# Optimization experiments

Measured on AMD Instinct MI355X. Metric: run time of the kernel, lower is better.

Reference implementation:

```python
import jax, jax.numpy as jnp
import numpy as np

B, T, H = 8, 2048, 2048


def _wkv(key, value, time_decay, time_first):
    # key, value: [B, T, H]; time_decay/time_first: [H]
    u = time_first
    w = -jnp.exp(time_decay)  # negative decay per channel

    a0 = jnp.zeros(key.shape[::2], key.dtype)            # [B, H]
    b0 = jnp.zeros_like(a0)
    e0 = jnp.full_like(a0, -jnp.inf)

    def step(carry, kv):
        a, b, exponent = carry
        kt, vt = kv                                       # [B, H] each
        # output for this timestep (numerically stabilized)
        max_exp = jnp.maximum(exponent, u + kt)
        wt = jnp.exp(u + kt - max_exp)
        scale = jnp.exp(exponent - max_exp)
        wkv = (a * scale + wt * vt) / (b * scale + wt)
        # state update with decay w
        max_exp2 = jnp.maximum(exponent + w, kt)
        s1 = jnp.exp(exponent + w - max_exp2)
        s2 = jnp.exp(kt - max_exp2)
        a = s1 * a + s2 * vt
        b = s1 * b + s2
        return (a, b, max_exp2), wkv

    kT = jnp.swapaxes(key, 0, 1)    # [T, B, H] for scan over time
    vT = jnp.swapaxes(value, 0, 1)
    _, out = jax.lax.scan(step, (a0, b0, e0), (kT, vT))
    return jnp.swapaxes(out, 0, 1)  # [B, T, H]


def setup_inputs() -> dict:
    key = jax.random.key(0)
    k1, k2, k3, k4 = jax.random.split(key, 4)
    return {
        "key": jax.random.normal(k1, (B, T, H), jnp.float32),
        "value": jax.random.normal(k2, (B, T, H), jnp.float32),
        "time_decay": jax.random.normal(k3, (H,), jnp.float32) * 0.5,
        "time_first": jax.random.normal(k4, (H,), jnp.float32) * 0.5,
    }


def reference(key, value, time_decay, time_first):
    return _wkv(key, value, time_decay, time_first)
```

## Files before the change

kernel.cpp:

```cpp
#include <hip/hip_runtime.h>
#include <math.h>


#define TT 2048
#define HH 2048
#define BHc 16384
#define H4 512
#define NGRP 8

struct __align__(16) f4 { float v[4]; };

__device__ __forceinline__ void upd1(float& a, float& b, float& e,
                                     float w, float k, float vv) {
    float ew = e + w;
    float m  = fmaxf(ew, k);
    float s1 = __expf(ew - m);
    float s2 = __expf(k - m);
    a = fmaf(s1, a, s2 * vv);
    b = fmaf(s1, b, s2);
    e = m;
}

__device__ __forceinline__ void compose(float& a, float& b, float& e,
                                        float qa, float qb, float qe, float dLw) {
    float ed = e + dLw;
    float m  = fmaxf(ed, qe);
    float s1 = __expf(ed - m);
    float s2 = __expf(qe - m);
    a = fmaf(s1, a, s2 * qa);
    b = fmaf(s1, b, s2 * qb);
    e = m;
}

template<int L>
__global__ __launch_bounds__(256, 4)
void wkv_pass1(const float* __restrict__ k_, const float* __restrict__ v_,
               const float* __restrict__ td,
               float* __restrict__ pa, float* __restrict__ pb,
               float* __restrict__ pe)
{
    const uint32_t t4  = blockIdx.x * 256u + threadIdx.x;
    const uint32_t c   = blockIdx.y;
    const uint32_t ch0 = t4 * 4u;
    const uint32_t h0  = ch0 & (HH - 1);
    const uint32_t b   = ch0 >> 11;

    const f4 wr = *(const f4*)(td + h0);
    float w[4], a[4], bs[4], e[4];
    #pragma unroll
    for (int j = 0; j < 4; ++j) {
        w[j] = -__expf(wr.v[j]); a[j] = 0.f; bs[j] = 0.f; e[j] = -INFINITY;
    }

    const uint32_t off4 = (b * (uint32_t)(TT * HH) + c * (uint32_t)(L * HH) + h0) >> 2;
    const f4* K4 = (const f4*)k_;
    const f4* V4 = (const f4*)v_;

    f4 kc = K4[off4], vc = V4[off4];
    #pragma unroll
    for (int t = 0; t < L; ++t) {
        f4 kn, vn;
        if (t + 1 < L) {
            kn = K4[off4 + (uint32_t)(t + 1) * H4];
            vn = V4[off4 + (uint32_t)(t + 1) * H4];
        }
        __builtin_amdgcn_sched_barrier(0);
        #pragma unroll
        for (int j = 0; j < 4; ++j) upd1(a[j], bs[j], e[j], w[j], kc.v[j], vc.v[j]);
        if (t + 1 < L) { kc = kn; vc = vn; }
    }

    const uint32_t pi4 = (c * (uint32_t)BHc + ch0) >> 2;
    f4 oa, ob, oe;
    #pragma unroll
    for (int j = 0; j < 4; ++j) { oa.v[j] = a[j]; ob.v[j] = bs[j]; oe.v[j] = e[j]; }
    ((f4*)pa)[pi4] = oa; ((f4*)pb)[pi4] = ob; ((f4*)pe)[pi4] = oe;
}

__global__ __launch_bounds__(256, 2)
void wkv_k2a(const float* __restrict__ pa, const float* __restrict__ pb,
             const float* __restrict__ pe,
             float* __restrict__ aa, float* __restrict__ ab,
             float* __restrict__ ae,
             const float* __restrict__ td, int CPG, int L)
{
    const uint32_t id = blockIdx.x * 256u + threadIdx.x;
    const uint32_t ch = id & (BHc - 1);
    const uint32_t g  = id >> 14;
    const float w  = -__expf(td[ch & (HH - 1)]);
    const float Lw = w * (float)L;

    float a = 0.f, b = 0.f, e = -INFINITY;
    for (int c = (int)g * CPG; c < (int)(g + 1) * CPG; ++c) {
        const uint32_t idx = (uint32_t)c * BHc + ch;
        compose(a, b, e, pa[idx], pb[idx], pe[idx], Lw);
    }
    const uint32_t gi = g * BHc + ch;
    aa[gi] = a; ab[gi] = b; ae[gi] = e;
}

__global__ __launch_bounds__(256, 2)
void wkv_k2b(float* __restrict__ aa, float* __restrict__ ab,
             float* __restrict__ ae, const float* __restrict__ td, int LC)
{
    const uint32_t ch = blockIdx.x * 256u + threadIdx.x;
    const float w   = -__expf(td[ch & (HH - 1)]);
    const float GLw = w * (float)LC;

    float a = 0.f, b = 0.f, e = -INFINITY;
    for (int g = 0; g < NGRP; ++g) {
        const uint32_t gi = (uint32_t)g * BHc + ch;
        float qa = aa[gi], qb = ab[gi], qe = ae[gi];
        aa[gi] = a; ab[gi] = b; ae[gi] = e;
        compose(a, b, e, qa, qb, qe, GLw);
    }
}

__global__ __launch_bounds__(256, 2)
void wkv_k2c(float* __restrict__ pa, float* __restrict__ pb,
             float* __restrict__ pe,
             const float* __restrict__ aa, const float* __restrict__ ab,
             const float* __restrict__ ae,
             const float* __restrict__ td, int CPG, int L)
{
    const uint32_t id = blockIdx.x * 256u + threadIdx.x;
    const uint32_t ch = id & (BHc - 1);
    const uint32_t g  = id >> 14;
    const float w  = -__expf(td[ch & (HH - 1)]);
    const float Lw = w * (float)L;

    const uint32_t gi = g * BHc + ch;
    float a = aa[gi], b = ab[gi], e = ae[gi];
    for (int c = (int)g * CPG; c < (int)(g + 1) * CPG; ++c) {
        const uint32_t idx = (uint32_t)c * BHc + ch;
        float qa = pa[idx], qb = pb[idx], qe = pe[idx];
        pa[idx] = a; pb[idx] = b; pe[idx] = e;
        compose(a, b, e, qa, qb, qe, Lw);
    }
}

template<int L>
__global__ __launch_bounds__(256, 4)
void wkv_pass3(const float* __restrict__ k_, const float* __restrict__ v_,
               const float* __restrict__ td, const float* __restrict__ tf,
               const float* __restrict__ pa, const float* __restrict__ pb,
               const float* __restrict__ pe,
               float* __restrict__ out)
{
    const uint32_t t4  = blockIdx.x * 256u + threadIdx.x;
    const uint32_t c   = blockIdx.y;
    const uint32_t ch0 = t4 * 4u;
    const uint32_t h0  = ch0 & (HH - 1);
    const uint32_t b   = ch0 >> 11;

    const f4 wr = *(const f4*)(td + h0);
    const f4 ur = *(const f4*)(tf + h0);
    const uint32_t pi4 = (c * (uint32_t)BHc + ch0) >> 2;
    const f4 ra = ((const f4*)pa)[pi4];
    const f4 rb = ((const f4*)pb)[pi4];
    const f4 re = ((const f4*)pe)[pi4];

    float w[4], u[4], a[4], bs[4], e[4];
    #pragma unroll
    for (int j = 0; j < 4; ++j) {
        w[j] = -__expf(wr.v[j]); u[j] = ur.v[j];
        a[j] = ra.v[j]; bs[j] = rb.v[j]; e[j] = re.v[j];
    }

    const uint32_t off4 = (b * (uint32_t)(TT * HH) + c * (uint32_t)(L * HH) + h0) >> 2;
    const f4* K4 = (const f4*)k_;
    const f4* V4 = (const f4*)v_;
    f4*       O4 = (f4*)out;

    f4 kc = K4[off4], vc = V4[off4];
    #pragma unroll
    for (int t = 0; t < L; ++t) {
        f4 kn, vn;
        if (t + 1 < L) {
            kn = K4[off4 + (uint32_t)(t + 1) * H4];
            vn = V4[off4 + (uint32_t)(t + 1) * H4];
        }
        __builtin_amdgcn_sched_barrier(0);
        f4 o;
        #pragma unroll
        for (int j = 0; j < 4; ++j) {
            float kt = kc.v[j], vt = vc.v[j];
            float uk  = u[j] + kt;
            float m   = fmaxf(e[j], uk);
            float wt  = __expf(uk - m);
            float sc  = __expf(e[j] - m);
            float num = fmaf(wt, vt, a[j] * sc);
            float den = fmaf(bs[j], sc, wt);
            o.v[j] = num * __builtin_amdgcn_rcpf(den);
            upd1(a[j], bs[j], e[j], w[j], kt, vt);
        }
        O4[off4 + (uint32_t)t * H4] = o;
        if (t + 1 < L) { kc = kn; vc = vn; }
    }
}

extern "C" void kernel_launch(void* const* d_in, const int* in_sizes, int n_in,
                              void* d_out, int out_size, void* d_ws, size_t ws_size,
                              hipStream_t stream) {
    const float* key   = (const float*)d_in[0];
    const float* value = (const float*)d_in[1];
    const float* td    = (const float*)d_in[2];
    const float* tf    = (const float*)d_in[3];
    float* out = (float*)d_out;

    int NC = 64;
    while (NC > 8 &&
           (size_t)3 * sizeof(float) * BHc * (NC + NGRP) > ws_size) NC >>= 1;
    const int L   = TT / NC;
    const int CPG = NC / NGRP;

    float* pa = (float*)d_ws;
    float* pb = pa + (size_t)BHc * NC;
    float* pe = pb + (size_t)BHc * NC;
    float* aa = pe + (size_t)BHc * NC;
    float* ab = aa + (size_t)BHc * NGRP;
    float* ae = ab + (size_t)BHc * NGRP;

    dim3 grid1(BHc / 4 / 256, NC);
    const int gk2 = BHc * NGRP / 256;
    const int gkb = BHc / 256;

    switch (L) {
    case 32:
        wkv_pass1<32><<<grid1, 256, 0, stream>>>(key, value, td, pa, pb, pe);
        break;
    case 64:
        wkv_pass1<64><<<grid1, 256, 0, stream>>>(key, value, td, pa, pb, pe);
        break;
    default:
        wkv_pass1<128><<<grid1, 256, 0, stream>>>(key, value, td, pa, pb, pe);
        break;
    }
    wkv_k2a<<<gk2, 256, 0, stream>>>(pa, pb, pe, aa, ab, ae, td, CPG, L);
    wkv_k2b<<<gkb, 256, 0, stream>>>(aa, ab, ae, td, L * CPG);
    wkv_k2c<<<gk2, 256, 0, stream>>>(pa, pb, pe, aa, ab, ae, td, CPG, L);
    switch (L) {
    case 32:
        wkv_pass3<32><<<grid1, 256, 0, stream>>>(key, value, td, tf, pa, pb, pe, out);
        break;
    case 64:
        wkv_pass3<64><<<grid1, 256, 0, stream>>>(key, value, td, tf, pa, pb, pe, out);
        break;
    default:
        wkv_pass3<128><<<grid1, 256, 0, stream>>>(key, value, td, tf, pa, pb, pe, out);
        break;
    }
}
```

Before: 414.1 us.

## Double chunk count, reshape pass grids, vectorize carry kernels, deepen prefetch

```diff
diff --git a/kernel.cpp b/kernel.cpp
--- a/kernel.cpp
+++ b/kernel.cpp
@@ -6,7 +6,8 @@
 #define HH 2048
 #define BHc 16384
 #define H4 512
-#define NGRP 8
+#define CH4 4096
+#define CPG 8
 
 struct __align__(16) f4 { float v[4]; };
 
@@ -33,17 +34,17 @@
 }
 
 template<int L>
-__global__ __launch_bounds__(256, 4)
+__global__ __launch_bounds__(512, 4)
 void wkv_pass1(const float* __restrict__ k_, const float* __restrict__ v_,
                const float* __restrict__ td,
                float* __restrict__ pa, float* __restrict__ pb,
                float* __restrict__ pe)
 {
-    const uint32_t t4  = blockIdx.x * 256u + threadIdx.x;
-    const uint32_t c   = blockIdx.y;
-    const uint32_t ch0 = t4 * 4u;
-    const uint32_t h0  = ch0 & (HH - 1);
-    const uint32_t b   = ch0 >> 11;
+    constexpr uint32_t NCk = TT / L;
+    const uint32_t tid = threadIdx.x;
+    const uint32_t b   = blockIdx.x / NCk;
+    const uint32_t c   = blockIdx.x % NCk;
+    const uint32_t h0  = tid * 4u;
 
     const f4 wr = *(const f4*)(td + h0);
     float w[4], a[4], bs[4], e[4];
@@ -52,29 +53,31 @@
         w[j] = -__expf(wr.v[j]); a[j] = 0.f; bs[j] = 0.f; e[j] = -INFINITY;
     }
 
-    const uint32_t off4 = (b * (uint32_t)(TT * HH) + c * (uint32_t)(L * HH) + h0) >> 2;
+    const uint32_t off4 = (b * (uint32_t)(TT * HH) + c * (uint32_t)(L * HH)) / 4u + tid;
     const f4* K4 = (const f4*)k_;
     const f4* V4 = (const f4*)v_;
 
-    f4 kc = K4[off4], vc = V4[off4];
+    f4 k0 = K4[off4],           v0 = V4[off4];
+    f4 k1 = K4[off4 + H4],      v1 = V4[off4 + H4];
     #pragma unroll
     for (int t = 0; t < L; ++t) {
-        f4 kn, vn;
-        if (t + 1 < L) {
-            kn = K4[off4 + (uint32_t)(t + 1) * H4];
-            vn = V4[off4 + (uint32_t)(t + 1) * H4];
+        f4 k2, v2;
+        if (t + 2 < L) {
+            k2 = K4[off4 + (uint32_t)(t + 2) * H4];
+            v2 = V4[off4 + (uint32_t)(t + 2) * H4];
         }
         __builtin_amdgcn_sched_barrier(0);
         #pragma unroll
-        for (int j = 0; j < 4; ++j) upd1(a[j], bs[j], e[j], w[j], kc.v[j], vc.v[j]);
-        if (t + 1 < L) { kc = kn; vc = vn; }
-    }
-
-    const uint32_t pi4 = (c * (uint32_t)BHc + ch0) >> 2;
+        for (int j = 0; j < 4; ++j) upd1(a[j], bs[j], e[j], w[j], k0.v[j], v0.v[j]);
+        k0 = k1; v0 = v1;
+        if (t + 2 < L) { k1 = k2; v1 = v2; }
+    }
+
+    const uint32_t p4 = (c * (uint32_t)BHc + b * (uint32_t)HH) / 4u + tid;
     f4 oa, ob, oe;
     #pragma unroll
     for (int j = 0; j < 4; ++j) { oa.v[j] = a[j]; ob.v[j] = bs[j]; oe.v[j] = e[j]; }
-    ((f4*)pa)[pi4] = oa; ((f4*)pb)[pi4] = ob; ((f4*)pe)[pi4] = oe;
+    ((f4*)pa)[p4] = oa; ((f4*)pb)[p4] = ob; ((f4*)pe)[p4] = oe;
 }
 
 __global__ __launch_bounds__(256, 2)
@@ -82,37 +85,64 @@
              const float* __restrict__ pe,
              float* __restrict__ aa, float* __restrict__ ab,
              float* __restrict__ ae,
-             const float* __restrict__ td, int CPG, int L)
-{
-    const uint32_t id = blockIdx.x * 256u + threadIdx.x;
-    const uint32_t ch = id & (BHc - 1);
-    const uint32_t g  = id >> 14;
-    const float w  = -__expf(td[ch & (HH - 1)]);
-    const float Lw = w * (float)L;
-
-    float a = 0.f, b = 0.f, e = -INFINITY;
+             const float* __restrict__ td, int L)
+{
+    const uint32_t id  = blockIdx.x * 256u + threadIdx.x;
+    const uint32_t ch4 = id & (CH4 - 1);
+    const uint32_t g   = id >> 12;
+    const uint32_t h0  = (ch4 * 4u) & (HH - 1);
+
+    const f4 wr = *(const f4*)(td + h0);
+    float Lw[4], a[4], b[4], e[4];
+    #pragma unroll
+    for (int j = 0; j < 4; ++j) {
+        Lw[j] = -__expf(wr.v[j]) * (float)L;
+        a[j] = 0.f; b[j] = 0.f; e[j] = -INFINITY;
+    }
+
     for (int c = (int)g * CPG; c < (int)(g + 1) * CPG; ++c) {
-        const uint32_t idx = (uint32_t)c * BHc + ch;
-        compose(a, b, e, pa[idx], pb[idx], pe[idx], Lw);
-    }
-    const uint32_t gi = g * BHc + ch;
-    aa[gi] = a; ab[gi] = b; ae[gi] = e;
+        const uint32_t i4 = (uint32_t)c * CH4 + ch4;
+        const f4 qa = ((const f4*)pa)[i4];
+        const f4 qb = ((const f4*)pb)[i4];
+        const f4 qe = ((const f4*)pe)[i4];
+        #pragma unroll
+        for (int j = 0; j < 4; ++j)
+            compose(a[j], b[j], e[j], qa.v[j], qb.v[j], qe.v[j], Lw[j]);
+    }
+    const uint32_t gi = g * CH4 + ch4;
+    f4 oa, ob, oe;
+    #pragma unroll
+    for (int j = 0; j < 4; ++j) { oa.v[j] = a[j]; ob.v[j] = b[j]; oe.v[j] = e[j]; }
+    ((f4*)aa)[gi] = oa; ((f4*)ab)[gi] = ob; ((f4*)ae)[gi] = oe;
 }
 
 __global__ __launch_bounds__(256, 2)
 void wkv_k2b(float* __restrict__ aa, float* __restrict__ ab,
-             float* __restrict__ ae, const float* __restrict__ td, int LC)
-{
-    const uint32_t ch = blockIdx.x * 256u + threadIdx.x;
-    const float w   = -__expf(td[ch & (HH - 1)]);
-    const float GLw = w * (float)LC;
-
-    float a = 0.f, b = 0.f, e = -INFINITY;
+             float* __restrict__ ae, const float* __restrict__ td,
+             int NGRP, int LC)
+{
+    const uint32_t ch4 = blockIdx.x * 256u + threadIdx.x;
+    const uint32_t h0  = (ch4 * 4u) & (HH - 1);
+    const f4 wr = *(const f4*)(td + h0);
+    float GLw[4], a[4], b[4], e[4];
+    #pragma unroll
+    for (int j = 0; j < 4; ++j) {
+        GLw[j] = -__expf(wr.v[j]) * (float)LC;
+        a[j] = 0.f; b[j] = 0.f; e[j] = -INFINITY;
+    }
+
     for (int g = 0; g < NGRP; ++g) {
-        const uint32_t gi = (uint32_t)g * BHc + ch;
-        float qa = aa[gi], qb = ab[gi], qe = ae[gi];
-        aa[gi] = a; ab[gi] = b; ae[gi] = e;
-        compose(a, b, e, qa, qb, qe, GLw);
+        const uint32_t gi = (uint32_t)g * CH4 + ch4;
+        const f4 qa = ((const f4*)aa)[gi];
+        const f4 qb = ((const f4*)ab)[gi];
+        const f4 qe = ((const f4*)ae)[gi];
+        f4 oa, ob, oe;
+        #pragma unroll
+        for (int j = 0; j < 4; ++j) { oa.v[j] = a[j]; ob.v[j] = b[j]; oe.v[j] = e[j]; }
+        ((f4*)aa)[gi] = oa; ((f4*)ab)[gi] = ob; ((f4*)ae)[gi] = oe;
+        #pragma unroll
+        for (int j = 0; j < 4; ++j)
+            compose(a[j], b[j], e[j], qa.v[j], qb.v[j], qe.v[j], GLw[j]);
     }
 }
 
@@ -121,44 +151,58 @@
              float* __restrict__ pe,
              const float* __restrict__ aa, const float* __restrict__ ab,
              const float* __restrict__ ae,
-             const float* __restrict__ td, int CPG, int L)
-{
-    const uint32_t id = blockIdx.x * 256u + threadIdx.x;
-    const uint32_t ch = id & (BHc - 1);
-    const uint32_t g  = id >> 14;
-    const float w  = -__expf(td[ch & (HH - 1)]);
-    const float Lw = w * (float)L;
-
-    const uint32_t gi = g * BHc + ch;
-    float a = aa[gi], b = ab[gi], e = ae[gi];
+             const float* __restrict__ td, int L)
+{
+    const uint32_t id  = blockIdx.x * 256u + threadIdx.x;
+    const uint32_t ch4 = id & (CH4 - 1);
+    const uint32_t g   = id >> 12;
+    const uint32_t h0  = (ch4 * 4u) & (HH - 1);
+
+    const f4 wr = *(const f4*)(td + h0);
+    const uint32_t gi = g * CH4 + ch4;
+    f4 ra = ((const f4*)aa)[gi], rb = ((const f4*)ab)[gi], re = ((const f4*)ae)[gi];
+    float Lw[4], a[4], b[4], e[4];
+    #pragma unroll
+    for (int j = 0; j < 4; ++j) {
+        Lw[j] = -__expf(wr.v[j]) * (float)L;
+        a[j] = ra.v[j]; b[j] = rb.v[j]; e[j] = re.v[j];
+    }
+
     for (int c = (int)g * CPG; c < (int)(g + 1) * CPG; ++c) {
-        const uint32_t idx = (uint32_t)c * BHc + ch;
-        float qa = pa[idx], qb = pb[idx], qe = pe[idx];
-        pa[idx] = a; pb[idx] = b; pe[idx] = e;
-        compose(a, b, e, qa, qb, qe, Lw);
+        const uint32_t i4 = (uint32_t)c * CH4 + ch4;
+        const f4 qa = ((const f4*)pa)[i4];
+        const f4 qb = ((const f4*)pb)[i4];
+        const f4 qe = ((const f4*)pe)[i4];
+        f4 oa, ob, oe;
+        #pragma unroll
+        for (int j = 0; j < 4; ++j) { oa.v[j] = a[j]; ob.v[j] = b[j]; oe.v[j] = e[j]; }
+        ((f4*)pa)[i4] = oa; ((f4*)pb)[i4] = ob; ((f4*)pe)[i4] = oe;
+        #pragma unroll
+        for (int j = 0; j < 4; ++j)
+            compose(a[j], b[j], e[j], qa.v[j], qb.v[j], qe.v[j], Lw[j]);
     }
 }
 
 template<int L>
-__global__ __launch_bounds__(256, 4)
+__global__ __launch_bounds__(512, 4)
 void wkv_pass3(const float* __restrict__ k_, const float* __restrict__ v_,
                const float* __restrict__ td, const float* __restrict__ tf,
                const float* __restrict__ pa, const float* __restrict__ pb,
                const float* __restrict__ pe,
                float* __restrict__ out)
 {
-    const uint32_t t4  = blockIdx.x * 256u + threadIdx.x;
-    const uint32_t c   = blockIdx.y;
-    const uint32_t ch0 = t4 * 4u;
-    const uint32_t h0  = ch0 & (HH - 1);
-    const uint32_t b   = ch0 >> 11;
+    constexpr uint32_t NCk = TT / L;
+    const uint32_t tid = threadIdx.x;
+    const uint32_t b   = blockIdx.x / NCk;
+    const uint32_t c   = blockIdx.x % NCk;
+    const uint32_t h0  = tid * 4u;
 
     const f4 wr = *(const f4*)(td + h0);
     const f4 ur = *(const f4*)(tf + h0);
-    const uint32_t pi4 = (c * (uint32_t)BHc + ch0) >> 2;
-    const f4 ra = ((const f4*)pa)[pi4];
-    const f4 rb = ((const f4*)pb)[pi4];
-    const f4 re = ((const f4*)pe)[pi4];
+    const uint32_t p4 = (c * (uint32_t)BHc + b * (uint32_t)HH) / 4u + tid;
+    const f4 ra = ((const f4*)pa)[p4];
+    const f4 rb = ((const f4*)pb)[p4];
+    const f4 re = ((const f4*)pe)[p4];
 
     float w[4], u[4], a[4], bs[4], e[4];
     #pragma unroll
@@ -167,24 +211,25 @@
         a[j] = ra.v[j]; bs[j] = rb.v[j]; e[j] = re.v[j];
     }
 
-    const uint32_t off4 = (b * (uint32_t)(TT * HH) + c * (uint32_t)(L * HH) + h0) >> 2;
+    const uint32_t off4 = (b * (uint32_t)(TT * HH) + c * (uint32_t)(L * HH)) / 4u + tid;
     const f4* K4 = (const f4*)k_;
     const f4* V4 = (const f4*)v_;
     f4*       O4 = (f4*)out;
 
-    f4 kc = K4[off4], vc = V4[off4];
+    f4 k0 = K4[off4],      v0 = V4[off4];
+    f4 k1 = K4[off4 + H4], v1 = V4[off4 + H4];
     #pragma unroll
     for (int t = 0; t < L; ++t) {
-        f4 kn, vn;
-        if (t + 1 < L) {
-            kn = K4[off4 + (uint32_t)(t + 1) * H4];
-            vn = V4[off4 + (uint32_t)(t + 1) * H4];
+        f4 k2, v2;
+        if (t + 2 < L) {
+            k2 = K4[off4 + (uint32_t)(t + 2) * H4];
+            v2 = V4[off4 + (uint32_t)(t + 2) * H4];
         }
         __builtin_amdgcn_sched_barrier(0);
         f4 o;
         #pragma unroll
         for (int j = 0; j < 4; ++j) {
-            float kt = kc.v[j], vt = vc.v[j];
+            float kt = k0.v[j], vt = v0.v[j];
             float uk  = u[j] + kt;
             float m   = fmaxf(e[j], uk);
             float wt  = __expf(uk - m);
@@ -195,7 +240,8 @@
             upd1(a[j], bs[j], e[j], w[j], kt, vt);
         }
         O4[off4 + (uint32_t)t * H4] = o;
-        if (t + 1 < L) { kc = kn; vc = vn; }
+        k0 = k1; v0 = v1;
+        if (t + 2 < L) { k1 = k2; v1 = v2; }
     }
 }
 
@@ -208,11 +254,11 @@
     const float* tf    = (const float*)d_in[3];
     float* out = (float*)d_out;
 
-    int NC = 64;
+    int NC = 128;
     while (NC > 8 &&
-           (size_t)3 * sizeof(float) * BHc * (NC + NGRP) > ws_size) NC >>= 1;
-    const int L   = TT / NC;
-    const int CPG = NC / NGRP;
+           (size_t)3 * sizeof(float) * BHc * (NC + NC / CPG) > ws_size) NC >>= 1;
+    const int L    = TT / NC;
+    const int NGRP = NC / CPG;
 
     float* pa = (float*)d_ws;
     float* pb = pa + (size_t)BHc * NC;
@@ -221,33 +267,33 @@
     float* ab = aa + (size_t)BHc * NGRP;
     float* ae = ab + (size_t)BHc * NGRP;
 
-    dim3 grid1(BHc / 4 / 256, NC);
-    const int gk2 = BHc * NGRP / 256;
-    const int gkb = BHc / 256;
+    const int gpass = 8 * NC;
+    const int g2    = CH4 * NGRP / 256;
+    const int g2b   = CH4 / 256;
 
     switch (L) {
+    case 16:
+        wkv_pass1<16><<<gpass, 512, 0, stream>>>(key, value, td, pa, pb, pe);
+        break;
     case 32:
-        wkv_pass1<32><<<grid1, 256, 0, stream>>>(key, value, td, pa, pb, pe);
-        break;
-    case 64:
-        wkv_pass1<64><<<grid1, 256, 0, stream>>>(key, value, td, pa, pb, pe);
+        wkv_pass1<32><<<gpass, 512, 0, stream>>>(key, value, td, pa, pb, pe);
         break;
     default:
-        wkv_pass1<128><<<grid1, 256, 0, stream>>>(key, value, td, pa, pb, pe);
-        break;
-    }
-    wkv_k2a<<<gk2, 256, 0, stream>>>(pa, pb, pe, aa, ab, ae, td, CPG, L);
-    wkv_k2b<<<gkb, 256, 0, stream>>>(aa, ab, ae, td, L * CPG);
-    wkv_k2c<<<gk2, 256, 0, stream>>>(pa, pb, pe, aa, ab, ae, td, CPG, L);
+        wkv_pass1<64><<<gpass, 512, 0, stream>>>(key, value, td, pa, pb, pe);
+        break;
+    }
+    wkv_k2a<<<g2, 256, 0, stream>>>(pa, pb, pe, aa, ab, ae, td, L);
+    wkv_k2b<<<g2b, 256, 0, stream>>>(aa, ab, ae, td, NGRP, L * CPG);
+    wkv_k2c<<<g2, 256, 0, stream>>>(pa, pb, pe, aa, ab, ae, td, L);
     switch (L) {
+    case 16:
+        wkv_pass3<16><<<gpass, 512, 0, stream>>>(key, value, td, tf, pa, pb, pe, out);
+        break;
     case 32:
-        wkv_pass3<32><<<grid1, 256, 0, stream>>>(key, value, td, tf, pa, pb, pe, out);
-        break;
-    case 64:
-        wkv_pass3<64><<<grid1, 256, 0, stream>>>(key, value, td, tf, pa, pb, pe, out);
+        wkv_pass3<32><<<gpass, 512, 0, stream>>>(key, value, td, tf, pa, pb, pe, out);
         break;
     default:
-        wkv_pass3<128><<<grid1, 256, 0, stream>>>(key, value, td, tf, pa, pb, pe, out);
-        break;
-    }
-}
+        wkv_pass3<64><<<gpass, 512, 0, stream>>>(key, value, td, tf, pa, pb, pe, out);
+        break;
+    }
+}
```

Result: faster. 399.0 us (-3.7%).
